# Optimization experiments

Hardware: AMD Instinct MI355X
Metric: run time of the kernel (lower is better)

## Reference

```python
import jax, jax.numpy as jnp
import numpy as np


def _safe_div(x, y):
    # avoid NaNs in branches that are masked out by jnp.where
    return x / jnp.where(jnp.abs(y) < 1e-12, 1.0, y)


def _closest_point_region(p, a, b, c):
    """Ericson closest-point-on-triangle, vectorized.
    p: [B,n,1,3]; a,b,c: [B,1,m,3] -> (dist2 [B,n,m], region [B,n,m] int32).
    Region codes: 0=vertA 1=vertB 2=vertC 3=edgeAB 4=edgeAC 5=edgeBC 6=face.
    """
    ab = b - a; ac = c - a; cb = c - b
    ap = p - a; bp = p - b; cp = p - c
    d1 = (ab * ap).sum(-1); d2 = (ac * ap).sum(-1)
    d3 = (ab * bp).sum(-1); d4 = (ac * bp).sum(-1)
    d5 = (ab * cp).sum(-1); d6 = (ac * cp).sum(-1)
    vc = d1 * d4 - d3 * d2
    vb = d5 * d2 - d1 * d6
    va = d3 * d6 - d5 * d4

    # candidate closest points per region
    v_ab = jnp.clip(_safe_div(d1, d1 - d3), 0.0, 1.0)
    v_ac = jnp.clip(_safe_div(d2, d2 - d6), 0.0, 1.0)
    v_bc = jnp.clip(_safe_div(d4 - d3, (d4 - d3) + (d5 - d6)), 0.0, 1.0)
    denom = va + vb + vc
    v_f = _safe_div(vb, denom); w_f = _safe_div(vc, denom)

    q_face = a + v_f[..., None] * ab + w_f[..., None] * ac
    q_ab = a + v_ab[..., None] * ab
    q_ac = a + v_ac[..., None] * ac
    q_bc = b + v_bc[..., None] * cb

    # region conditions (Ericson priority: a, b, ab, c, ac, bc, face)
    cond_a = (d1 <= 0) & (d2 <= 0)
    cond_b = (d3 >= 0) & (d4 <= d3)
    cond_ab = (vc <= 0) & (d1 >= 0) & (d3 <= 0)
    cond_c = (d6 >= 0) & (d5 <= d6)
    cond_ac = (vb <= 0) & (d2 >= 0) & (d6 <= 0)
    cond_bc = (va <= 0) & (d4 - d3 >= 0) & (d5 - d6 >= 0)

    def sel(cond, qc, code, q, region):
        q = jnp.where(cond[..., None], qc, q)
        region = jnp.where(cond, code, region)
        return q, region

    # apply lowest priority first so higher-priority regions overwrite
    q = q_face
    region = jnp.full(q.shape[:-1], 6, dtype=jnp.int32)
    q, region = sel(cond_bc, q_bc, 5, q, region)
    q, region = sel(cond_ac, q_ac, 4, q, region)
    q, region = sel(cond_c, c, 2, q, region)
    q, region = sel(cond_ab, q_ab, 3, q, region)
    q, region = sel(cond_b, b, 1, q, region)
    q, region = sel(cond_a, a, 0, q, region)

    diff = p - q
    dist2 = (diff * diff).sum(-1)  # squared distance, as in chamfer-style kernels
    return dist2, region


def setup_inputs() -> dict:
    key = jax.random.key(0)
    k1, k2, k3, k4 = jax.random.split(key, 4)
    B, n, m = 4, 4096, 512
    xyz1 = jax.random.normal(k1, (B, n, 3), dtype=jnp.float32)
    tri1 = jax.random.normal(k2, (B, m, 3), dtype=jnp.float32)
    tri2 = jax.random.normal(k3, (B, m, 3), dtype=jnp.float32)
    tri3 = jax.random.normal(k4, (B, m, 3), dtype=jnp.float32)
    return {"xyz1": xyz1, "tri1": tri1, "tri2": tri2, "tri3": tri3}


def reference(xyz1, tri1, tri2, tri3):
    p = xyz1[:, :, None, :]       # [B,n,1,3]
    a = tri1[:, None, :, :]       # [B,1,m,3]
    b = tri2[:, None, :, :]
    c = tri3[:, None, :, :]
    dist2, region = _closest_point_region(p, a, b, c)  # [B,n,m]
    index = jnp.argmin(dist2, axis=-1).astype(jnp.int32)            # [B,n]
    dist = jnp.min(dist2, axis=-1)                                  # [B,n]
    point = jnp.take_along_axis(region, index[..., None].astype(jnp.int64), axis=-1)[..., 0]
    return dist, point, index
```

## Files before the change

kernel.cpp:

```cpp
#include <hip/hip_runtime.h>
#include <math.h>

#define BB 4
#define NN 4096
#define MM 512
#define PTS 8
#define NPT 4
#define CHUNKS 64
#define MCHUNK (MM / CHUNKS)
#define TPB 512

typedef float v2 __attribute__((ext_vector_type(2)));

__device__ __forceinline__ v2 pfma(v2 a, v2 b, v2 c) {
    return __builtin_elementwise_fma(a, b, c);
}
__device__ __forceinline__ v2 pmin(v2 a, v2 b) { return __builtin_elementwise_min(a, b); }
__device__ __forceinline__ v2 pmax(v2 a, v2 b) { return __builtin_elementwise_max(a, b); }
__device__ __forceinline__ v2 pclip01(v2 x) { return pmin(pmax(x, (v2)0.0f), (v2)1.0f); }

__device__ __forceinline__ float safercp(float y) {
    float yy = (fabsf(y) < 1e-12f) ? 1.0f : y;
    return __builtin_amdgcn_rcpf(yy);
}

__device__ __forceinline__ float safediv(float x, float y) {
    float yy = (fabsf(y) < 1e-12f) ? 1.0f : y;
    return x / yy;
}

__device__ __forceinline__ float clip01s(float x) {
    return fminf(fmaxf(x, 0.0f), 1.0f);
}

__device__ void exact_pair(float px, float py, float pz,
                           float ax, float ay, float az,
                           float bx, float by, float bz,
                           float cx, float cy, float cz,
                           float* dist2_out, int* reg_out) {
#pragma clang fp contract(off)
    const float abx = bx-ax, aby = by-ay, abz = bz-az;
    const float acx = cx-ax, acy = cy-ay, acz = cz-az;
    const float cbx = cx-bx, cby = cy-by, cbz = cz-bz;
    const float apx = px-ax, apy = py-ay, apz = pz-az;
    const float bpx = px-bx, bpy = py-by, bpz = pz-bz;
    const float cpx = px-cx, cpy = py-cy, cpz = pz-cz;

    const float d1 = abx*apx + aby*apy + abz*apz;
    const float d2 = acx*apx + acy*apy + acz*apz;
    const float d3 = abx*bpx + aby*bpy + abz*bpz;
    const float d4 = acx*bpx + acy*bpy + acz*bpz;
    const float d5 = abx*cpx + aby*cpy + abz*cpz;
    const float d6 = acx*cpx + acy*cpy + acz*cpz;

    const float vc = d1*d4 - d3*d2;
    const float vb = d5*d2 - d1*d6;
    const float va = d3*d6 - d5*d4;

    const float v_ab = clip01s(safediv(d1, d1 - d3));
    const float v_ac = clip01s(safediv(d2, d2 - d6));
    const float t43 = d4 - d3;
    const float t56 = d5 - d6;
    const float v_bc = clip01s(safediv(t43, t43 + t56));
    const float denom = va + vb + vc;
    const float v_f = safediv(vb, denom);
    const float w_f = safediv(vc, denom);

    float qx = ax + v_f*abx + w_f*acx;
    float qy = ay + v_f*aby + w_f*acy;
    float qz = az + v_f*abz + w_f*acz;
    int reg = 6;
    const bool c_bc = (va <= 0.0f) && (t43 >= 0.0f) && (t56 >= 0.0f);
    if (c_bc) { qx = bx + v_bc*cbx; qy = by + v_bc*cby; qz = bz + v_bc*cbz; reg = 5; }
    const bool c_ac = (vb <= 0.0f) && (d2 >= 0.0f) && (d6 <= 0.0f);
    if (c_ac) { qx = ax + v_ac*acx; qy = ay + v_ac*acy; qz = az + v_ac*acz; reg = 4; }
    const bool c_c = (d6 >= 0.0f) && (d5 <= d6);
    if (c_c) { qx = cx; qy = cy; qz = cz; reg = 2; }
    const bool c_ab = (vc <= 0.0f) && (d1 >= 0.0f) && (d3 <= 0.0f);
    if (c_ab) { qx = ax + v_ab*abx; qy = ay + v_ab*aby; qz = az + v_ab*abz; reg = 3; }
    const bool c_b = (d3 >= 0.0f) && (d4 <= d3);
    if (c_b) { qx = bx; qy = by; qz = bz; reg = 1; }
    const bool c_a = (d1 <= 0.0f) && (d2 <= 0.0f);
    if (c_a) { qx = ax; qy = ay; qz = az; reg = 0; }

    const float dx = px - qx;
    const float dy = py - qy;
    const float dz = pz - qz;
    *dist2_out = dx*dx + dy*dy + dz*dz;
    *reg_out = reg;
}

__global__ __launch_bounds__(TPB) void tridist_kernel(
    const float* __restrict__ xyz1, const float* __restrict__ tri1,
    const float* __restrict__ tri2, const float* __restrict__ tri3,
    float* __restrict__ out)
{
    __shared__ float4 sT[(MM / 8) * 49];
    __shared__ float  sPd[NPT][64];
    __shared__ int    sPj[NPT][64];

    const int t  = threadIdx.x;
    const int b  = blockIdx.x >> 7;
    const int pb = blockIdx.x & 127;
    const int pt = t & (PTS - 1);
    const int ch = t >> 3;

    {
        const int jj = t;
        const float* g1 = tri1 + ((size_t)b * MM + jj) * 3;
        const float* g2 = tri2 + ((size_t)b * MM + jj) * 3;
        const float* g3 = tri3 + ((size_t)b * MM + jj) * 3;
        const float ax = g1[0], ay = g1[1], az = g1[2];
        const float bx = g2[0], by = g2[1], bz = g2[2];
        const float cx = g3[0], cy = g3[1], cz = g3[2];
        const float abx = bx-ax, aby = by-ay, abz = bz-az;
        const float acx = cx-ax, acy = cy-ay, acz = cz-az;
        const float cbx = cx-bx, cby = cy-by, cbz = cz-bz;
        const float aba  = fmaf(abz, az, fmaf(aby, ay, abx*ax));
        const float aca  = fmaf(acz, az, fmaf(acy, ay, acx*ax));
        const float ab2  = fmaf(abz, abz, fmaf(aby, aby, abx*abx));
        const float ac2  = fmaf(acz, acz, fmaf(acy, acy, acx*acx));
        const float cb2  = fmaf(cbz, cbz, fmaf(cby, cby, cbx*cbx));
        const float abac = fmaf(abz, acz, fmaf(aby, acy, abx*acx));
        const float nrx = fmaf(aby, acz, -(abz*acy));
        const float nry = fmaf(abz, acx, -(abx*acz));
        const float nrz = fmaf(abx, acy, -(aby*acx));
        const float n2  = fmaf(nrz, nrz, fmaf(nry, nry, nrx*nrx));
        const float rn  = __builtin_amdgcn_rsqf(fmaxf(n2, 1e-30f));
        const float nx = nrx*rn, ny = nry*rn, nz = nrz*rn;
        const float nna = -fmaf(nz, az, fmaf(ny, ay, nx*ax));
        const int base = (jj >> 3) * 49 + (jj & 7) * 6;
        sT[base + 0] = make_float4(ax, ay, az, nna);
        sT[base + 1] = make_float4(abx, aby, abz, safercp(ab2));
        sT[base + 2] = make_float4(acx, acy, acz, safercp(ac2));
        sT[base + 3] = make_float4(cbx, cby, cbz, safercp(cb2));
        sT[base + 4] = make_float4(nx, ny, nz, abac);
        sT[base + 5] = make_float4(-aba, -aca, ab2, ac2);
    }
    __syncthreads();

    v2 Px[2], Py[2], Pz[2];
#pragma unroll
    for (int np = 0; np < NPT; ++np) {
        const int gi = b * NN + pb * 32 + np * PTS + pt;
        Px[np >> 1][np & 1] = xyz1[gi*3 + 0];
        Py[np >> 1][np & 1] = xyz1[gi*3 + 1];
        Pz[np >> 1][np & 1] = xyz1[gi*3 + 2];
    }

    float bestd[NPT] = {INFINITY, INFINITY, INFINITY, INFINITY};
    int   bestj[NPT] = {0, 0, 0, 0};

    for (int i = 0; i < MCHUNK; ++i) {
        const int j = ch * MCHUNK + i;
        const int base = ch * 49 + i * 6;
        const float4 r0 = sT[base + 0];
        const float4 r1 = sT[base + 1];
        const float4 r2 = sT[base + 2];
        const float4 r3 = sT[base + 3];
        const float4 r4 = sT[base + 4];
        const float4 r5 = sT[base + 5];
        const float ax = r0.x, ay = r0.y, az = r0.z, nna = r0.w;
        const float abx = r1.x, aby = r1.y, abz = r1.z, rab2 = r1.w;
        const float acx = r2.x, acy = r2.y, acz = r2.z, rac2 = r2.w;
        const float cbx = r3.x, cby = r3.y, cbz = r3.z, rcb2 = r3.w;
        const float nx = r4.x, ny = r4.y, nz = r4.z, abac = r4.w;
        const float naba = r5.x, naca = r5.y, ab2 = r5.z, ac2 = r5.w;

#pragma unroll
        for (int g = 0; g < 2; ++g) {
            const v2 X = Px[g], Y = Py[g], Z = Pz[g];

            const v2 d1 = pfma((v2)abz, Z, pfma((v2)aby, Y, pfma((v2)abx, X, (v2)naba)));
            const v2 d2 = pfma((v2)acz, Z, pfma((v2)acy, Y, pfma((v2)acx, X, (v2)naca)));
            const v2 h  = pfma((v2)nz,  Z, pfma((v2)ny,  Y, pfma((v2)nx,  X, (v2)nna)));
            const v2 d3 = d1 - (v2)ab2;
            const v2 d4 = d2 - (v2)abac;
            const v2 d5 = d1 - (v2)abac;
            const v2 d6 = d2 - (v2)ac2;

            const v2 vc = pfma(d1, d4, -(d3*d2));
            const v2 vb = pfma(d5, d2, -(d1*d6));
            const v2 va = pfma(d3, d6, -(d5*d4));
            const v2 t43 = d4 - d3;

            const v2 v_ab = pclip01(d1 * (v2)rab2);
            const v2 v_ac = pclip01(d2 * (v2)rac2);
            const v2 v_bc = pclip01(t43 * (v2)rcb2);

            const v2 apx = X - (v2)ax, apy = Y - (v2)ay, apz = Z - (v2)az;
            const v2 bpx = apx - (v2)abx, bpy = apy - (v2)aby, bpz = apz - (v2)abz;

            v2 ex = pfma(-v_ab, (v2)abx, apx);
            v2 ey = pfma(-v_ab, (v2)aby, apy);
            v2 ez = pfma(-v_ab, (v2)abz, apz);
            const v2 dAB = pfma(ez, ez, pfma(ey, ey, ex*ex));
            ex = pfma(-v_ac, (v2)acx, apx);
            ey = pfma(-v_ac, (v2)acy, apy);
            ez = pfma(-v_ac, (v2)acz, apz);
            const v2 dAC = pfma(ez, ez, pfma(ey, ey, ex*ex));
            ex = pfma(-v_bc, (v2)cbx, bpx);
            ey = pfma(-v_bc, (v2)cby, bpy);
            ez = pfma(-v_bc, (v2)cbz, bpz);
            const v2 dBC = pfma(ez, ez, pfma(ey, ey, ex*ex));
            const v2 dF = h * h;

            const v2 mv   = pmin(pmin(va, vb), vc);
            const v2 dseg = pmin(pmin(dAB, dAC), dBC);

#pragma unroll
            for (int c = 0; c < 2; ++c) {
                const float dist2 = (mv[c] >= 0.0f) ? dF[c] : dseg[c];
                const int np = g * 2 + c;
                if (dist2 < bestd[np]) { bestd[np] = dist2; bestj[np] = j; }
            }
        }
    }

#pragma unroll
    for (int np = 0; np < NPT; ++np) {
        for (int off = 8; off <= 32; off <<= 1) {
            const float od = __shfl_xor(bestd[np], off, 64);
            const int   oj = __shfl_xor(bestj[np], off, 64);
            if (od < bestd[np] || (od == bestd[np] && oj < bestj[np])) {
                bestd[np] = od; bestj[np] = oj;
            }
        }
    }
    const int lane = t & 63;
    const int w    = t >> 6;
    if (lane < PTS) {
#pragma unroll
        for (int np = 0; np < NPT; ++np) {
            sPd[np][w * PTS + lane] = bestd[np];
            sPj[np][w * PTS + lane] = bestj[np];
        }
    }
    __syncthreads();

    if (t < 32) {
        const int np = t >> 3;
        const int p  = t & 7;
        float bd = INFINITY; int bj = 0;
        for (int k = 0; k < 8; ++k) {
            const float dk = sPd[np][k * PTS + p];
            const int   jk = sPj[np][k * PTS + p];
            if (dk < bd || (dk == bd && jk < bj)) { bd = dk; bj = jk; }
        }
        const float* g1 = tri1 + ((size_t)b * MM + bj) * 3;
        const float* g2 = tri2 + ((size_t)b * MM + bj) * 3;
        const float* g3 = tri3 + ((size_t)b * MM + bj) * 3;
        const int gidx = b * NN + pb * 32 + t;
        float dist2; int reg;
        exact_pair(xyz1[gidx*3+0], xyz1[gidx*3+1], xyz1[gidx*3+2],
                   g1[0], g1[1], g1[2],
                   g2[0], g2[1], g2[2],
                   g3[0], g3[1], g3[2],
                   &dist2, &reg);
        out[gidx]             = dist2;
        out[BB*NN + gidx]     = (float)reg;
        out[2*BB*NN + gidx]   = (float)bj;
    }
}

extern "C" void kernel_launch(void* const* d_in, const int* in_sizes, int n_in,
                              void* d_out, int out_size, void* d_ws, size_t ws_size,
                              hipStream_t stream) {
    const float* xyz1 = (const float*)d_in[0];
    const float* tri1 = (const float*)d_in[1];
    const float* tri2 = (const float*)d_in[2];
    const float* tri3 = (const float*)d_in[3];
    float* out = (float*)d_out;

    dim3 grid(BB * (NN / 32));
    dim3 block(TPB);
    tridist_kernel<<<grid, block, 0, stream>>>(xyz1, tri1, tri2, tri3, out);
}
```

Baseline: 72.16 us.

## Split triangle range across two blocks and merge with a second kernel

The triangle set is split into two halves, each handled by a separate block, which doubles the grid to 1024 blocks. Each block writes its per-point best distance and index to workspace. A second kernel picks the better half and runs the exact closest-point computation. The intent is more blocks for better occupancy across the CUs and half the shared-memory setup per block, paid for with an extra kernel launch and a round trip through workspace. Ties go to the lower index because j0 always comes from the lower half.

Measured after the change: 130.0 us. 1.8x slower.

```diff
diff --git a/kernel.cpp b/kernel.cpp
--- a/kernel.cpp
+++ b/kernel.cpp
@@ -4,11 +4,12 @@
 #define BB 4
 #define NN 4096
 #define MM 512
+#define MH (MM / 2)
 #define PTS 8
 #define NPT 4
-#define CHUNKS 64
-#define MCHUNK (MM / CHUNKS)
+#define MCHUNK (MH / 64)
 #define TPB 512
+#define NPTS_TOT (BB * NN)
 
 typedef float v2 __attribute__((ext_vector_type(2)));
 
@@ -90,26 +91,29 @@
     *reg_out = reg;
 }
 
-__global__ __launch_bounds__(TPB) void tridist_kernel(
+__global__ __launch_bounds__(TPB, 8) void tridist_p1(
     const float* __restrict__ xyz1, const float* __restrict__ tri1,
     const float* __restrict__ tri2, const float* __restrict__ tri3,
-    float* __restrict__ out)
+    float* __restrict__ wd, int* __restrict__ wj)
 {
-    __shared__ float4 sT[(MM / 8) * 49];
+    __shared__ float4 sT[(MH / 8) * 49];
     __shared__ float  sPd[NPT][64];
     __shared__ int    sPj[NPT][64];
 
-    const int t  = threadIdx.x;
-    const int b  = blockIdx.x >> 7;
-    const int pb = blockIdx.x & 127;
-    const int pt = t & (PTS - 1);
-    const int ch = t >> 3;
-
-    {
+    const int t    = threadIdx.x;
+    const int half = blockIdx.x & 1;
+    const int bp   = blockIdx.x >> 1;
+    const int b    = bp >> 7;
+    const int pb   = bp & 127;
+    const int pt   = t & (PTS - 1);
+    const int ch   = t >> 3;
+    const int jbase = half * MH;
+
+    if (t < MH) {
         const int jj = t;
-        const float* g1 = tri1 + ((size_t)b * MM + jj) * 3;
-        const float* g2 = tri2 + ((size_t)b * MM + jj) * 3;
-        const float* g3 = tri3 + ((size_t)b * MM + jj) * 3;
+        const float* g1 = tri1 + ((size_t)b * MM + jbase + jj) * 3;
+        const float* g2 = tri2 + ((size_t)b * MM + jbase + jj) * 3;
+        const float* g3 = tri3 + ((size_t)b * MM + jbase + jj) * 3;
         const float ax = g1[0], ay = g1[1], az = g1[2];
         const float bx = g2[0], by = g2[1], bz = g2[2];
         const float cx = g3[0], cy = g3[1], cz = g3[2];
@@ -152,8 +156,8 @@
     int   bestj[NPT] = {0, 0, 0, 0};
 
     for (int i = 0; i < MCHUNK; ++i) {
-        const int j = ch * MCHUNK + i;
-        const int base = ch * 49 + i * 6;
+        const int lj = ch * MCHUNK + i;
+        const int base = (lj >> 3) * 49 + (lj & 7) * 6;
         const float4 r0 = sT[base + 0];
         const float4 r1 = sT[base + 1];
         const float4 r2 = sT[base + 2];
@@ -212,7 +216,7 @@
             for (int c = 0; c < 2; ++c) {
                 const float dist2 = (mv[c] >= 0.0f) ? dF[c] : dseg[c];
                 const int np = g * 2 + c;
-                if (dist2 < bestd[np]) { bestd[np] = dist2; bestj[np] = j; }
+                if (dist2 < bestd[np]) { bestd[np] = dist2; bestj[np] = jbase + lj; }
             }
         }
     }
@@ -247,20 +251,38 @@
             const int   jk = sPj[np][k * PTS + p];
             if (dk < bd || (dk == bd && jk < bj)) { bd = dk; bj = jk; }
         }
-        const float* g1 = tri1 + ((size_t)b * MM + bj) * 3;
-        const float* g2 = tri2 + ((size_t)b * MM + bj) * 3;
-        const float* g3 = tri3 + ((size_t)b * MM + bj) * 3;
         const int gidx = b * NN + pb * 32 + t;
-        float dist2; int reg;
-        exact_pair(xyz1[gidx*3+0], xyz1[gidx*3+1], xyz1[gidx*3+2],
-                   g1[0], g1[1], g1[2],
-                   g2[0], g2[1], g2[2],
-                   g3[0], g3[1], g3[2],
-                   &dist2, &reg);
-        out[gidx]             = dist2;
-        out[BB*NN + gidx]     = (float)reg;
-        out[2*BB*NN + gidx]   = (float)bj;
-    }
+        wd[half * NPTS_TOT + gidx] = bd;
+        wj[half * NPTS_TOT + gidx] = bj;
+    }
+}
+
+__global__ __launch_bounds__(256) void tridist_p2(
+    const float* __restrict__ xyz1, const float* __restrict__ tri1,
+    const float* __restrict__ tri2, const float* __restrict__ tri3,
+    const float* __restrict__ wd, const int* __restrict__ wj,
+    float* __restrict__ out)
+{
+    const int gidx = blockIdx.x * 256 + threadIdx.x;
+    const float d0 = wd[gidx];
+    const float d1 = wd[NPTS_TOT + gidx];
+    const int   j0 = wj[gidx];
+    const int   j1 = wj[NPTS_TOT + gidx];
+    const int bj = (d1 < d0) ? j1 : j0;
+
+    const int b = gidx >> 12;
+    const float* g1 = tri1 + ((size_t)b * MM + bj) * 3;
+    const float* g2 = tri2 + ((size_t)b * MM + bj) * 3;
+    const float* g3 = tri3 + ((size_t)b * MM + bj) * 3;
+    float dist2; int reg;
+    exact_pair(xyz1[gidx*3+0], xyz1[gidx*3+1], xyz1[gidx*3+2],
+               g1[0], g1[1], g1[2],
+               g2[0], g2[1], g2[2],
+               g3[0], g3[1], g3[2],
+               &dist2, &reg);
+    out[gidx]               = dist2;
+    out[NPTS_TOT + gidx]    = (float)reg;
+    out[2*NPTS_TOT + gidx]  = (float)bj;
 }
 
 extern "C" void kernel_launch(void* const* d_in, const int* in_sizes, int n_in,
@@ -272,7 +294,12 @@
     const float* tri3 = (const float*)d_in[3];
     float* out = (float*)d_out;
 
-    dim3 grid(BB * (NN / 32));
-    dim3 block(TPB);
-    tridist_kernel<<<grid, block, 0, stream>>>(xyz1, tri1, tri2, tri3, out);
-}
+    float* wd = (float*)d_ws;
+    int*   wj = (int*)((char*)d_ws + 2 * NPTS_TOT * sizeof(float));
+
+    dim3 grid1(BB * (NN / 32) * 2);
+    tridist_p1<<<grid1, TPB, 0, stream>>>(xyz1, tri1, tri2, tri3, wd, wj);
+
+    dim3 grid2(NPTS_TOT / 256);
+    tridist_p2<<<grid2, 256, 0, stream>>>(xyz1, tri1, tri2, tri3, wd, wj, out);
+}
```
